# Performance work log

Hardware: AMD Instinct MI355X
Metric: run time of the kernel (lower is better)

Reference implementation:

```python
import jax, jax.numpy as jnp
import numpy as np

K = 4            # number of candidate kernels in Dynamic_conv2d
TEMP = 34.0      # softmax temperature (default in Dynamic_conv2d)
C = 64           # channel


def _dyn_conv(x, w, fc1_w, fc2_w, fc2_b, pad, dil):
    """Dynamic_conv2d forward.
    x: [B,Cin,H,W]; w: [K,Cout,Cin,k,k]; fc1_w: [hid,Cin]; fc2_w: [K,hid]; fc2_b: [K].
    """
    pooled = x.mean(axis=(2, 3))                                   # [B,Cin] adaptive avg pool
    h = jax.nn.relu(jnp.einsum('bc,hc->bh', pooled, fc1_w))        # [B,hid]
    logits = jnp.einsum('bh,kh->bk', h, fc2_w) + fc2_b             # [B,K]
    att = jax.nn.softmax(logits / TEMP, axis=-1)                   # [B,K]
    agg_w = jnp.einsum('bk,koihw->boihw', att, w)                  # per-sample kernel [B,Cout,Cin,k,k]

    def conv_one(xi, wi):
        return jax.lax.conv_general_dilated(
            xi[None], wi, window_strides=(1, 1),
            padding=[(pad, pad), (pad, pad)], rhs_dilation=(dil, dil),
            dimension_numbers=('NCHW', 'OIHW', 'NCHW'))[0]

    return jax.vmap(conv_one)(x, agg_w)                            # [B,Cout,H,W]


def _leaky(v):
    return jnp.where(v >= 0, v, 0.1 * v)


def _mk_params(key, cin, cout):
    hid = int(cin * 0.25) + 1
    k1, k2, k3, k4 = jax.random.split(key, 4)
    scale = np.sqrt(2.0 / (cin * 9)).astype(np.float32)
    w = jax.random.normal(k1, (K, cout, cin, 3, 3), jnp.float32) * scale
    fc1 = jax.random.normal(k2, (hid, cin), jnp.float32) * np.sqrt(2.0 / cin).astype(np.float32)
    fc2w = jax.random.normal(k3, (K, hid), jnp.float32) * np.sqrt(2.0 / hid).astype(np.float32)
    fc2b = jnp.zeros((K,), jnp.float32)
    return w, fc1, fc2w, fc2b


def setup_inputs() -> dict:
    key = jax.random.key(0)
    ks = jax.random.split(key, 5)
    x = jax.random.normal(ks[0], (16, C, 128, 128), jnp.float32)
    out = {'x': x}
    for i, (kk, cin) in enumerate(zip(ks[1:4], [C, C, C]), start=1):
        w, fc1, fc2w, fc2b = _mk_params(kk, cin, C)
        out[f'w{i}'], out[f'fc1_{i}'], out[f'fc2w_{i}'], out[f'fc2b_{i}'] = w, fc1, fc2w, fc2b
    w, fc1, fc2w, fc2b = _mk_params(ks[4], 3 * C, C)
    out['wt'], out['fc1_t'], out['fc2w_t'], out['fc2b_t'] = w, fc1, fc2w, fc2b
    return out


def reference(x, w1, fc1_1, fc2w_1, fc2b_1, w2, fc1_2, fc2w_2, fc2b_2,
              w3, fc1_3, fc2w_3, fc2b_3, wt, fc1_t, fc2w_t, fc2b_t):
    b1 = _leaky(_dyn_conv(x, w1, fc1_1, fc2w_1, fc2b_1, pad=1, dil=1))
    b2 = _leaky(_dyn_conv(x, w2, fc1_2, fc2w_2, fc2b_2, pad=2, dil=2))
    b3 = _leaky(_dyn_conv(x, w3, fc1_3, fc2w_3, fc2b_3, pad=4, dil=4))
    cat = jnp.concatenate([b1, b2, b3], axis=1)                    # [B,3C,H,W]
    return x + _dyn_conv(cat, wt, fc1_t, fc2w_t, fc2b_t, pad=1, dil=1)
```

## Files before the change

kernel.cpp:

```cpp
#include <hip/hip_runtime.h>
#include <hip/hip_bf16.h>

typedef __hip_bfloat16 bf16;
typedef __attribute__((ext_vector_type(4))) float f32x4;
typedef __attribute__((ext_vector_type(8))) short bf16x8;
typedef __attribute__((ext_vector_type(4))) short s16x4;

#define BB 16
#define HH 128
#define WW 128
#define HWSZ (HH*WW)
#define XH 136
#define XW 136
#define XPAD 4
#define CHH 130
#define CWD 130
#define CPAD 1
#define CATC 192

__device__ __forceinline__ void zero_border_body(bf16* __restrict__ base, int HP, int WP,
                                                 int PAD, int Cdim, int slots)
{
    int cg8 = Cdim >> 3;
    int per_b = slots * cg8;
    int idx = blockIdx.x * 256 + threadIdx.x;
    if (idx >= BB * per_b) return;
    int b = idx / per_b;
    int rem = idx - b * per_b;
    int slot = rem / cg8;
    int cg = rem - slot * cg8;
    int top = PAD * WP;
    int h, w;
    if (slot < top)            { h = slot / WP;            w = slot % WP; }
    else if (slot < 2 * top)   { int s = slot - top;       h = HP - PAD + s / WP; w = s % WP; }
    else {
        int s = slot - 2 * top;
        int row = s / (2 * PAD), t = s - row * (2 * PAD);
        h = PAD + row;
        w = (t < PAD) ? t : (WP - 2 * PAD + t);
    }
    bf16x8 z = {0,0,0,0,0,0,0,0};
    *(bf16x8*)(base + (((size_t)b * HP + h) * WP + w) * Cdim + cg * 8) = z;
}

__global__ void init_borders(bf16* __restrict__ xT, bf16* __restrict__ catT,
                             float* __restrict__ pooledx, float* __restrict__ pooledc)
{
    if (blockIdx.y == 0) {
        if (blockIdx.x == 0) {
            for (int i = threadIdx.x; i < BB * 64;   i += 256) pooledx[i] = 0.f;
            for (int i = threadIdx.x; i < BB * CATC; i += 256) pooledc[i] = 0.f;
        }
        zero_border_body(xT,   XH,  XW,  XPAD, 64,   2112);
    } else {
        zero_border_body(catT, CHH, CWD, CPAD, CATC, 516);
    }
}

__global__ __launch_bounds__(256)
void transpose_pad_pool_x(const float* __restrict__ x, bf16* __restrict__ xT,
                          float* __restrict__ pooledx)
{
    __shared__ float tile[128 * 65];
    const int h = blockIdx.x, b = blockIdx.y;
    const int t = threadIdx.x;
    const int w  = t & 127;
    const int chalf = t >> 7;

    const float* xb = x + (((size_t)b * 64) * HH + h) * WW + w;
    #pragma unroll
    for (int it = 0; it < 32; ++it) {
        int c = it * 2 + chalf;
        tile[w * 65 + c] = xb[(size_t)c * HWSZ];
    }
    __syncthreads();

    bf16* dst = xT + (((size_t)b * XH + (h + XPAD)) * XW + XPAD) * 64;
    #pragma unroll
    for (int it = 0; it < 4; ++it) {
        int v  = t + it * 256;
        int ww = v >> 3;
        int c0 = (v & 7) * 8;
        const float* src = tile + ww * 65 + c0;
        bf16x8 pk;
        #pragma unroll
        for (int j = 0; j < 8; ++j)
            pk[j] = __builtin_bit_cast(short, __float2bfloat16(src[j]));
        *(bf16x8*)(dst + (size_t)ww * 64 + c0) = pk;
    }

    if (t < 64) {
        float s = 0.f;
        #pragma unroll 4
        for (int ww = 0; ww < 128; ++ww) s += tile[ww * 65 + t];
        atomicAdd(pooledx + b * 64 + t, s);
    }
}

__device__ __forceinline__ void attn_body(int b, const float* pooled, int Cin,
                                          const float* fc1, int hid,
                                          const float* fc2w, const float* fc2b,
                                          float* att, float* sp, float* sh, float* slg)
{
    for (int c = threadIdx.x; c < Cin; c += 64) sp[c] = pooled[b * Cin + c];
    __syncthreads();
    int j = threadIdx.x;
    if (j < hid) {
        float s = 0.f;
        const float4* f4 = (const float4*)(fc1 + (size_t)j * Cin);
        for (int c4 = 0; c4 < Cin / 4; ++c4) {
            float4 v = f4[c4];
            s += v.x * sp[c4*4+0] + v.y * sp[c4*4+1] + v.z * sp[c4*4+2] + v.w * sp[c4*4+3];
        }
        sh[j] = s > 0.f ? s * (1.0f / 16384.0f) : 0.f;
    }
    __syncthreads();
    int k = threadIdx.x;
    if (k < 4) {
        float s = fc2b[k];
        for (int jj = 0; jj < hid; ++jj) s += fc2w[k * hid + jj] * sh[jj];
        slg[k] = s * (1.0f / 34.0f);
    }
    __syncthreads();
    if (threadIdx.x == 0) {
        float m = fmaxf(fmaxf(slg[0], slg[1]), fmaxf(slg[2], slg[3]));
        float e0 = expf(slg[0]-m), e1 = expf(slg[1]-m), e2 = expf(slg[2]-m), e3 = expf(slg[3]-m);
        float inv = 1.0f / (e0+e1+e2+e3);
        att[b*4+0] = e0*inv; att[b*4+1] = e1*inv; att[b*4+2] = e2*inv; att[b*4+3] = e3*inv;
    }
}

__global__ void attention3(const float* __restrict__ pooled,
                           const float* f1a, const float* f2a, const float* ba, float* aa,
                           const float* f1b, const float* f2b, const float* bb, float* ab,
                           const float* f1c, const float* f2c, const float* bc, float* ac)
{
    __shared__ float sp[192], sh[64], slg[4];
    int br = blockIdx.y;
    const float* fc1  = br == 0 ? f1a : br == 1 ? f1b : f1c;
    const float* fc2w = br == 0 ? f2a : br == 1 ? f2b : f2c;
    const float* fc2b = br == 0 ? ba  : br == 1 ? bb  : bc;
    float* att        = br == 0 ? aa  : br == 1 ? ab  : ac;
    attn_body(blockIdx.x, pooled, 64, fc1, 17, fc2w, fc2b, att, sp, sh, slg);
}

__global__ void attention_one(const float* __restrict__ pooled, int Cin,
                              const float* __restrict__ fc1, int hid,
                              const float* __restrict__ fc2w,
                              const float* __restrict__ fc2b, float* __restrict__ att)
{
    __shared__ float sp[192], sh[64], slg[4];
    attn_body(blockIdx.x, pooled, Cin, fc1, hid, fc2w, fc2b, att, sp, sh, slg);
}

template<int CIN, bool PERM>
__device__ __forceinline__ void aggw_body(const float* __restrict__ w,
                                          const float* __restrict__ att,
                                          bf16* __restrict__ out, float* wl)
{
    constexpr int C9 = CIN * 9;
    constexpr int NS = (CIN / 32) * 9;
    const int co = blockIdx.x, b = blockIdx.y;
    const int src = PERM ? ((co & 15) * 4 + (co >> 4)) : co;
    for (int i = threadIdx.x; i < 4 * C9; i += 256) {
        int k = i / C9, rem = i - k * C9;
        wl[i] = w[((size_t)k * 64 + src) * C9 + rem];
    }
    __syncthreads();
    float a0 = att[b*4+0], a1 = att[b*4+1], a2 = att[b*4+2], a3 = att[b*4+3];
    const int m = co >> 4, l15 = co & 15;
    char* ob = (char*)out + (size_t)b * NS * 4096;
    for (int t = threadIdx.x; t < NS * 32; t += 256) {
        int s = t >> 5, rem = t & 31;
        int gg = rem >> 3, j = rem & 7;
        int chunk = s / 9, tap = s - chunk * 9;
        int ci = chunk * 32 + gg * 8 + j;
        float v = a0 * wl[ci*9 + tap] + a1 * wl[C9 + ci*9 + tap]
                + a2 * wl[2*C9 + ci*9 + tap] + a3 * wl[3*C9 + ci*9 + tap];
        *(bf16*)(ob + ((size_t)((s*4 + m) * 64 + (gg*16 + l15))) * 16 + j * 2) = __float2bfloat16(v);
    }
}

__global__ void aggw_frag3(const float* __restrict__ w1, const float* __restrict__ att1, bf16* o1,
                           const float* __restrict__ w2, const float* __restrict__ att2, bf16* o2,
                           const float* __restrict__ w3, const float* __restrict__ att3, bf16* o3)
{
    __shared__ float wl[4 * 64 * 9];
    int z = blockIdx.z;
    if (z == 0)      aggw_body<64, true>(w1, att1, o1, wl);
    else if (z == 1) aggw_body<64, true>(w2, att2, o2, wl);
    else             aggw_body<64, true>(w3, att3, o3, wl);
}

__global__ void aggw_frag_t(const float* __restrict__ w, const float* __restrict__ att,
                            bf16* __restrict__ out)
{
    __shared__ float wl[4 * 192 * 9];
    aggw_body<192, false>(w, att, out, wl);
}

template<int DIL, int CIN>
__device__ __forceinline__ void conv_core(
    int b, int hb, int wt,
    const bf16* __restrict__ inT, int HPd, int WPd, int PAD,
    const bf16* __restrict__ aggwF,
    bf16* __restrict__ catT, int catbase, float* __restrict__ poolc,
    char* lds, float* sco)
{
    constexpr int NCHUNK = CIN / 32;
    constexpr int SLOTS  = 64 + 2 * DIL;
    constexpr int ROWB   = SLOTS * 64;
    constexpr int XBYTES = 10 * ROWB;
    constexpr int XSEG   = (XBYTES + 1023) / 1024;
    constexpr int ABYTES = 36864;
    constexpr int MAXT   = (XSEG + 7) / 8;

    const int r  = hb % DIL;
    const int q  = hb / DIL;
    const int tid  = threadIdx.x;
    const int wv   = tid >> 6;
    const int lane = tid & 63;
    const int n16  = lane & 15;
    const int g    = lane >> 4;

    const char* inB = (const char*)inT;
    const char* awB = (const char*)aggwF + (size_t)b * (NCHUNK * ABYTES);

    if (tid < 64) sco[tid] = 0.f;

    int baddr[12];
    #pragma unroll
    for (int nt = 0; nt < 4; ++nt)
        #pragma unroll
        for (int kw = 0; kw < 3; ++kw)
            baddr[nt*3+kw] = wv * ROWB + g * (SLOTS * 16)
                             + (nt * 16 + n16 + kw * DIL) * 16;

    int xoff[MAXT];
    #pragma unroll
    for (int t = 0; t < MAXT; ++t) {
        int i = wv + 8 * t;
        xoff[t] = 0;
        if (i < XSEG) {
            int o = i * 1024 + lane * 16;
            if (o < XBYTES) {
                int row  = o / ROWB;
                int rem  = o - row * ROWB;
                int g2   = rem / (SLOTS * 16);
                int slot = (rem - g2 * (SLOTS * 16)) >> 4;
                int h_in = (q * 8 + row - 1) * DIL + r;
                xoff[t] = ((b * HPd + PAD + h_in) * WPd + (PAD + wt * 64 - DIL + slot)) * (CIN * 2)
                          + g2 * 16;
            }
        }
    }

    auto stage = [&](int c) {
        #pragma unroll
        for (int t = 0; t < MAXT; ++t) {
            int i = wv + 8 * t;
            if (i >= XSEG) break;
            __builtin_amdgcn_global_load_lds(
                (const __attribute__((address_space(1))) void*)(inB + (size_t)(xoff[t] + c * 64)),
                (__attribute__((address_space(3))) void*)(lds + i * 1024), 16, 0, 0);
        }
    };

    f32x4 acc[4][4];
    #pragma unroll
    for (int nt = 0; nt < 4; ++nt)
        #pragma unroll
        for (int m = 0; m < 4; ++m) { f32x4 z = {0.f,0.f,0.f,0.f}; acc[nt][m] = z; }

    for (int c = 0; c < NCHUNK; ++c) {
        stage(c);
        __syncthreads();
        const char* awC = awB + (size_t)c * ABYTES + (size_t)lane * 16;
        #pragma unroll 3
        for (int tap = 0; tap < 9; ++tap) {
            const int kh = tap / 3, kw = tap - kh * 3;
            bf16x8 a[4];
            #pragma unroll
            for (int m = 0; m < 4; ++m)
                a[m] = *(const bf16x8*)(awC + (size_t)((tap * 4 + m) * 1024));
            #pragma unroll
            for (int nt = 0; nt < 4; ++nt) {
                const bf16x8 bfr = *(const bf16x8*)(lds + baddr[nt * 3 + kw] + kh * ROWB);
                #pragma unroll
                for (int m = 0; m < 4; ++m)
                    acc[nt][m] = __builtin_amdgcn_mfma_f32_16x16x32_bf16(a[m], bfr, acc[nt][m], 0, 0, 0);
            }
        }
        __syncthreads();
    }

    const int h_out = (q * 8 + wv) * DIL + r;
    float csum[4][4];
    #pragma unroll
    for (int m = 0; m < 4; ++m)
        #pragma unroll
        for (int qq = 0; qq < 4; ++qq) csum[m][qq] = 0.f;
    #pragma unroll
    for (int nt = 0; nt < 4; ++nt) {
        int w_out = wt * 64 + nt * 16 + n16;
        char* dst = (char*)(catT + (((size_t)b * CHH + (CPAD + h_out)) * CWD + (CPAD + w_out)) * CATC
                            + catbase) + g * 32;
        float lv[4][4];
        #pragma unroll
        for (int m = 0; m < 4; ++m)
            #pragma unroll
            for (int qq = 0; qq < 4; ++qq) {
                float v = acc[nt][m][qq];
                v = v >= 0.f ? v : 0.1f * v;
                lv[m][qq] = v;
                csum[m][qq] += v;
            }
        bf16x8 lo, hi;
        #pragma unroll
        for (int j = 0; j < 8; ++j) {
            lo[j] = __builtin_bit_cast(short, __float2bfloat16(lv[j & 3][j >> 2]));
            hi[j] = __builtin_bit_cast(short, __float2bfloat16(lv[j & 3][2 + (j >> 2)]));
        }
        *(bf16x8*)(dst)      = lo;
        *(bf16x8*)(dst + 16) = hi;
    }
    #pragma unroll
    for (int m = 0; m < 4; ++m)
        #pragma unroll
        for (int qq = 0; qq < 4; ++qq) {
            float v = csum[m][qq];
            v += __shfl_xor(v, 1, 64);
            v += __shfl_xor(v, 2, 64);
            v += __shfl_xor(v, 4, 64);
            v += __shfl_xor(v, 8, 64);
            if (n16 == 0) atomicAdd(&sco[g * 16 + qq * 4 + m], v);
        }
    __syncthreads();
    if (tid < 64) atomicAdd(poolc + b * CATC + catbase + tid, sco[tid]);
}

__global__ __launch_bounds__(512, 4)
void conv_branch3(const bf16* __restrict__ xT,
                  const bf16* __restrict__ aggF1, const bf16* __restrict__ aggF2,
                  const bf16* __restrict__ aggF3,
                  bf16* __restrict__ catT, float* __restrict__ poolc)
{
    constexpr int SCOO = 46080;
    __shared__ __align__(1024) char lds[SCOO + 256];
    float* sco = (float*)(lds + SCOO);

    const int bid  = blockIdx.x;
    const int xcd  = bid & 7;
    const int j    = bid >> 3;
    const int b    = 2 * xcd + (j >= 96 ? 1 : 0);
    const int u    = j % 96;
    const int band = u / 24;
    const int v    = u % 24;
    const int br   = v % 3;
    const int t2   = v / 3;
    const int wt   = t2 & 1;
    const int hb   = band * 4 + (t2 >> 1);

    if (br == 0)
        conv_core<1, 64>(b, hb, wt, xT, XH, XW, XPAD, aggF1, catT, 0,   poolc, lds, sco);
    else if (br == 1)
        conv_core<2, 64>(b, hb, wt, xT, XH, XW, XPAD, aggF2, catT, 64,  poolc, lds, sco);
    else
        conv_core<4, 64>(b, hb, wt, xT, XH, XW, XPAD, aggF3, catT, 128, poolc, lds, sco);
}

#define FF_ROWB 4224
#define FF_XBY  25344
#define FF_XSEG 25

__global__ __launch_bounds__(256, 4)
void conv_final(const bf16* __restrict__ catT, const bf16* __restrict__ aggFt,
                const float* __restrict__ x, float* __restrict__ out)
{
    __shared__ __align__(1024) char lds[FF_XSEG * 1024];

    const int bid = blockIdx.x;
    const int xcd = bid & 7;
    const int j   = bid >> 3;
    const int b   = 2 * xcd + (j >= 64 ? 1 : 0);
    const int u   = j & 63;
    const int wt  = u & 1;
    const int hb  = u >> 1;

    const int tid  = threadIdx.x;
    const int wv   = tid >> 6;
    const int lane = tid & 63;
    const int n16  = lane & 15;
    const int g    = lane >> 4;

    const char* inB = (const char*)catT;
    const char* awB = (const char*)aggFt + (size_t)b * (6 * 36864);

    int baddr[12];
    #pragma unroll
    for (int nt = 0; nt < 4; ++nt)
        #pragma unroll
        for (int kw = 0; kw < 3; ++kw)
            baddr[nt*3+kw] = wv * FF_ROWB + g * (66 * 16) + (nt * 16 + n16 + kw) * 16;

    int xoff[7];
    #pragma unroll
    for (int t = 0; t < 7; ++t) {
        int i = wv + 4 * t;
        xoff[t] = 0;
        if (i < FF_XSEG) {
            int o = i * 1024 + lane * 16;
            if (o < FF_XBY) {
                int row  = o / FF_ROWB;
                int rem  = o - row * FF_ROWB;
                int g2   = rem / (66 * 16);
                int slot = (rem - g2 * (66 * 16)) >> 4;
                int h_in = hb * 4 + row - 1;
                xoff[t] = ((b * CHH + CPAD + h_in) * CWD + (CPAD + wt * 64 - 1 + slot)) * (CATC * 2)
                          + g2 * 16;
            }
        }
    }

    auto stage = [&](int c) {
        #pragma unroll
        for (int t = 0; t < 7; ++t) {
            int i = wv + 4 * t;
            if (i >= FF_XSEG) break;
            __builtin_amdgcn_global_load_lds(
                (const __attribute__((address_space(1))) void*)(inB + (size_t)(xoff[t] + c * 64)),
                (__attribute__((address_space(3))) void*)(lds + i * 1024), 16, 0, 0);
        }
    };

    f32x4 acc[4][4];
    #pragma unroll
    for (int nt = 0; nt < 4; ++nt)
        #pragma unroll
        for (int m = 0; m < 4; ++m) { f32x4 z = {0.f,0.f,0.f,0.f}; acc[nt][m] = z; }

    for (int c = 0; c < 6; ++c) {
        stage(c);
        __syncthreads();
        const char* awC = awB + (size_t)c * 36864 + (size_t)lane * 16;
        #pragma unroll 3
        for (int tap = 0; tap < 9; ++tap) {
            const int kh = tap / 3, kw = tap - kh * 3;
            bf16x8 a[4];
            #pragma unroll
            for (int m = 0; m < 4; ++m)
                a[m] = *(const bf16x8*)(awC + (size_t)((tap * 4 + m) * 1024));
            #pragma unroll
            for (int nt = 0; nt < 4; ++nt) {
                const bf16x8 bfr = *(const bf16x8*)(lds + baddr[nt * 3 + kw] + kh * FF_ROWB);
                #pragma unroll
                for (int m = 0; m < 4; ++m)
                    acc[nt][m] = __builtin_amdgcn_mfma_f32_16x16x32_bf16(a[m], bfr, acc[nt][m], 0, 0, 0);
            }
        }
        __syncthreads();
    }

    const int h_out = hb * 4 + wv;
    #pragma unroll
    for (int nt = 0; nt < 4; ++nt) {
        int w_out = wt * 64 + nt * 16 + n16;
        #pragma unroll
        for (int m = 0; m < 4; ++m) {
            int co = m * 16 + g * 4;
            size_t base = (((size_t)b * 64 + co) * HH + h_out) * WW + w_out;
            #pragma unroll
            for (int qq = 0; qq < 4; ++qq) {
                size_t idx = base + (size_t)qq * HWSZ;
                out[idx] = x[idx] + acc[nt][m][qq];
            }
        }
    }
}

extern "C" void kernel_launch(void* const* d_in, const int* in_sizes, int n_in,
                              void* d_out, int out_size, void* d_ws, size_t ws_size,
                              hipStream_t stream) {
    const float* x      = (const float*)d_in[0];
    const float* w1     = (const float*)d_in[1];
    const float* fc1_1  = (const float*)d_in[2];
    const float* fc2w_1 = (const float*)d_in[3];
    const float* fc2b_1 = (const float*)d_in[4];
    const float* w2     = (const float*)d_in[5];
    const float* fc1_2  = (const float*)d_in[6];
    const float* fc2w_2 = (const float*)d_in[7];
    const float* fc2b_2 = (const float*)d_in[8];
    const float* w3     = (const float*)d_in[9];
    const float* fc1_3  = (const float*)d_in[10];
    const float* fc2w_3 = (const float*)d_in[11];
    const float* fc2b_3 = (const float*)d_in[12];
    const float* wt     = (const float*)d_in[13];
    const float* fc1_t  = (const float*)d_in[14];
    const float* fc2w_t = (const float*)d_in[15];
    const float* fc2b_t = (const float*)d_in[16];
    float* out = (float*)d_out;
    (void)in_sizes; (void)n_in; (void)out_size; (void)ws_size;

    char* ws = (char*)d_ws;
    auto alloc = [&](size_t bytes) { char* p = ws; ws += (bytes + 255) & ~(size_t)255; return p; };

    bf16*  aggF1   = (bf16*)alloc((size_t)BB * 18 * 4096);
    bf16*  aggF2   = (bf16*)alloc((size_t)BB * 18 * 4096);
    bf16*  aggF3   = (bf16*)alloc((size_t)BB * 18 * 4096);
    bf16*  aggFt   = (bf16*)alloc((size_t)BB * 54 * 4096);
    float* pooledx = (float*)alloc(BB * 64 * 4);
    float* pooledc = (float*)alloc(BB * 192 * 4);
    float* att1    = (float*)alloc(BB * 4 * 4);
    float* att2    = (float*)alloc(BB * 4 * 4);
    float* att3    = (float*)alloc(BB * 4 * 4);
    float* attt    = (float*)alloc(BB * 4 * 4);
    alloc(65536);
    const size_t XT_BYTES  = (size_t)BB * XH * XW * 64 * 2;
    bf16* xT   = (bf16*)alloc(XT_BYTES);
    alloc(65536);
    const size_t CAT_BYTES = (size_t)BB * CHH * CWD * CATC * 2;
    bf16* catT = (bf16*)alloc(CAT_BYTES);
    alloc(65536);

    init_borders<<<dim3(1056, 2), 256, 0, stream>>>(xT, catT, pooledx, pooledc);

    transpose_pad_pool_x<<<dim3(128, 16), 256, 0, stream>>>(x, xT, pooledx);

    attention3<<<dim3(16, 3), 64, 0, stream>>>(pooledx,
        fc1_1, fc2w_1, fc2b_1, att1,
        fc1_2, fc2w_2, fc2b_2, att2,
        fc1_3, fc2w_3, fc2b_3, att3);

    aggw_frag3<<<dim3(64, 16, 3), 256, 0, stream>>>(w1, att1, aggF1,
                                                    w2, att2, aggF2,
                                                    w3, att3, aggF3);

    conv_branch3<<<1536, 512, 0, stream>>>(xT, aggF1, aggF2, aggF3, catT, pooledc);

    attention_one<<<16, 64, 0, stream>>>(pooledc, CATC, fc1_t, 49, fc2w_t, fc2b_t, attt);
    aggw_frag_t<<<dim3(64, 16), 256, 0, stream>>>(wt, attt, aggFt);

    conv_final<<<1024, 256, 0, stream>>>(catT, aggFt, x, out);
}
```

Before: 230.8 us.

## Compute two output rows per wave in final conv to reuse weight and input fragments

Each wave of the final conv now computes two output rows instead of one, so the block covers 8 rows and the grid is halved. Input rows are staged once into a larger LDS tile (10 rows). Per kernel column the 3x4 weight fragments and 4 row fragments are loaded once and reused across both output rows. This cuts global weight loads and LDS reads per MFMA, at the cost of doubling the accumulator registers (launch bounds reduced to 2 blocks per CU) and using more LDS.

```diff
diff --git a/kernel.cpp b/kernel.cpp
--- a/kernel.cpp
+++ b/kernel.cpp
@@ -370,10 +370,10 @@
 }
 
 #define FF_ROWB 4224
-#define FF_XBY  25344
-#define FF_XSEG 25
-
-__global__ __launch_bounds__(256, 4)
+#define FF_XBY  42240
+#define FF_XSEG 42
+
+__global__ __launch_bounds__(256, 2)
 void conv_final(const bf16* __restrict__ catT, const bf16* __restrict__ aggFt,
                 const float* __restrict__ x, float* __restrict__ out)
 {
@@ -382,8 +382,8 @@
     const int bid = blockIdx.x;
     const int xcd = bid & 7;
     const int j   = bid >> 3;
-    const int b   = 2 * xcd + (j >= 64 ? 1 : 0);
-    const int u   = j & 63;
+    const int b   = 2 * xcd + (j >= 32 ? 1 : 0);
+    const int u   = j & 31;
     const int wt  = u & 1;
     const int hb  = u >> 1;
 
@@ -401,11 +401,11 @@
     for (int nt = 0; nt < 4; ++nt)
         #pragma unroll
         for (int kw = 0; kw < 3; ++kw)
-            baddr[nt*3+kw] = wv * FF_ROWB + g * (66 * 16) + (nt * 16 + n16 + kw) * 16;
-
-    int xoff[7];
-    #pragma unroll
-    for (int t = 0; t < 7; ++t) {
+            baddr[nt*3+kw] = (2 * wv) * FF_ROWB + g * (66 * 16) + (nt * 16 + n16 + kw) * 16;
+
+    int xoff[11];
+    #pragma unroll
+    for (int t = 0; t < 11; ++t) {
         int i = wv + 4 * t;
         xoff[t] = 0;
         if (i < FF_XSEG) {
@@ -415,7 +415,7 @@
                 int rem  = o - row * FF_ROWB;
                 int g2   = rem / (66 * 16);
                 int slot = (rem - g2 * (66 * 16)) >> 4;
-                int h_in = hb * 4 + row - 1;
+                int h_in = hb * 8 + row - 1;
                 xoff[t] = ((b * CHH + CPAD + h_in) * CWD + (CPAD + wt * 64 - 1 + slot)) * (CATC * 2)
                           + g2 * 16;
             }
@@ -424,7 +424,7 @@
 
     auto stage = [&](int c) {
         #pragma unroll
-        for (int t = 0; t < 7; ++t) {
+        for (int t = 0; t < 11; ++t) {
             int i = wv + 4 * t;
             if (i >= FF_XSEG) break;
             __builtin_amdgcn_global_load_lds(
@@ -433,46 +433,60 @@
         }
     };
 
-    f32x4 acc[4][4];
-    #pragma unroll
-    for (int nt = 0; nt < 4; ++nt)
-        #pragma unroll
-        for (int m = 0; m < 4; ++m) { f32x4 z = {0.f,0.f,0.f,0.f}; acc[nt][m] = z; }
+    f32x4 acc[2][4][4];
+    #pragma unroll
+    for (int orr = 0; orr < 2; ++orr)
+        #pragma unroll
+        for (int nt = 0; nt < 4; ++nt)
+            #pragma unroll
+            for (int m = 0; m < 4; ++m) { f32x4 z = {0.f,0.f,0.f,0.f}; acc[orr][nt][m] = z; }
 
     for (int c = 0; c < 6; ++c) {
         stage(c);
         __syncthreads();
         const char* awC = awB + (size_t)c * 36864 + (size_t)lane * 16;
-        #pragma unroll 3
-        for (int tap = 0; tap < 9; ++tap) {
-            const int kh = tap / 3, kw = tap - kh * 3;
-            bf16x8 a[4];
-            #pragma unroll
-            for (int m = 0; m < 4; ++m)
-                a[m] = *(const bf16x8*)(awC + (size_t)((tap * 4 + m) * 1024));
-            #pragma unroll
-            for (int nt = 0; nt < 4; ++nt) {
-                const bf16x8 bfr = *(const bf16x8*)(lds + baddr[nt * 3 + kw] + kh * FF_ROWB);
+        #pragma unroll
+        for (int kw = 0; kw < 3; ++kw) {
+            bf16x8 a[3][4];
+            #pragma unroll
+            for (int kh = 0; kh < 3; ++kh)
                 #pragma unroll
                 for (int m = 0; m < 4; ++m)
-                    acc[nt][m] = __builtin_amdgcn_mfma_f32_16x16x32_bf16(a[m], bfr, acc[nt][m], 0, 0, 0);
+                    a[kh][m] = *(const bf16x8*)(awC + (size_t)(((kh * 3 + kw) * 4 + m) * 1024));
+            #pragma unroll
+            for (int nt = 0; nt < 4; ++nt) {
+                bf16x8 bfr[4];
+                #pragma unroll
+                for (int rr = 0; rr < 4; ++rr)
+                    bfr[rr] = *(const bf16x8*)(lds + baddr[nt * 3 + kw] + rr * FF_ROWB);
+                #pragma unroll
+                for (int kh = 0; kh < 3; ++kh)
+                    #pragma unroll
+                    for (int orr = 0; orr < 2; ++orr)
+                        #pragma unroll
+                        for (int m = 0; m < 4; ++m)
+                            acc[orr][nt][m] = __builtin_amdgcn_mfma_f32_16x16x32_bf16(
+                                a[kh][m], bfr[orr + kh], acc[orr][nt][m], 0, 0, 0);
             }
         }
         __syncthreads();
     }
 
-    const int h_out = hb * 4 + wv;
-    #pragma unroll
-    for (int nt = 0; nt < 4; ++nt) {
-        int w_out = wt * 64 + nt * 16 + n16;
-        #pragma unroll
-        for (int m = 0; m < 4; ++m) {
-            int co = m * 16 + g * 4;
-            size_t base = (((size_t)b * 64 + co) * HH + h_out) * WW + w_out;
-            #pragma unroll
-            for (int qq = 0; qq < 4; ++qq) {
-                size_t idx = base + (size_t)qq * HWSZ;
-                out[idx] = x[idx] + acc[nt][m][qq];
+    #pragma unroll
+    for (int orr = 0; orr < 2; ++orr) {
+        const int h_out = hb * 8 + 2 * wv + orr;
+        #pragma unroll
+        for (int nt = 0; nt < 4; ++nt) {
+            int w_out = wt * 64 + nt * 16 + n16;
+            #pragma unroll
+            for (int m = 0; m < 4; ++m) {
+                int co = m * 16 + g * 4;
+                size_t base = (((size_t)b * 64 + co) * HH + h_out) * WW + w_out;
+                #pragma unroll
+                for (int qq = 0; qq < 4; ++qq) {
+                    size_t idx = base + (size_t)qq * HWSZ;
+                    out[idx] = x[idx] + acc[orr][nt][m][qq];
+                }
             }
         }
     }
@@ -540,5 +554,5 @@
     attention_one<<<16, 64, 0, stream>>>(pooledc, CATC, fc1_t, 49, fc2w_t, fc2b_t, attt);
     aggw_frag_t<<<dim3(64, 16), 256, 0, stream>>>(wt, attt, aggFt);
 
-    conv_final<<<1024, 256, 0, stream>>>(catT, aggFt, x, out);
-}
+    conv_final<<<512, 256, 0, stream>>>(catT, aggFt, x, out);
+}
```

Result: faster. 219.3 us (-5.0%).
